# Kernel optimization log

Hardware: AMD Instinct MI355X
Metric: run time of the kernel (lower is better)

The kernel has to match this reference:

```python
import jax, jax.numpy as jnp
import numpy as np

WINDOW_SIZE = 2
SOFTMAX_TEMP = 0.01
CART_RESOLUTION = 0.25
RANGE_KEEP = 3.0
EPS = 1e-12


def get_indices(batch_size, window_size):
    kp, dense = [], []
    for i in range(batch_size):
        for j in range(window_size - 1):
            kp.append(i * window_size + j)
            dense.append(i * window_size + j + 1)
    return np.asarray(kp), np.asarray(dense)


def normalize_coords(coords, height, width):
    # coords [B,N,2] pixel (u,v) -> [-1,1] (align_corners=True convention, as in the repo)
    u = 2.0 * coords[..., 0] / (width - 1) - 1.0
    v = 2.0 * coords[..., 1] / (height - 1) - 1.0
    return jnp.stack([u, v], axis=-1)


def grid_sample_bilinear(img, grid):
    # Matches torch F.grid_sample(mode='bilinear', padding_mode='zeros', align_corners=False)
    # img [B,C,H,W], grid [B,Hg,Wg,2] with (x,y) in [-1,1]
    B, C, H, W = img.shape
    x = ((grid[..., 0] + 1.0) * W - 1.0) * 0.5
    y = ((grid[..., 1] + 1.0) * H - 1.0) * 0.5
    x0 = jnp.floor(x); y0 = jnp.floor(y)
    wx1 = x - x0; wy1 = y - y0

    def gather(xi, yi):
        valid = (xi >= 0) & (xi <= W - 1) & (yi >= 0) & (yi <= H - 1)
        xc = jnp.clip(xi, 0, W - 1).astype(jnp.int32)
        yc = jnp.clip(yi, 0, H - 1).astype(jnp.int32)
        v = jax.vmap(lambda im, yy, xx: im[:, yy, xx])(img, yc, xc)  # [B,C,Hg,Wg]
        return v * valid[:, None].astype(img.dtype)

    x1 = x0 + 1.0; y1 = y0 + 1.0
    out = (gather(x0, y0) * ((1.0 - wx1) * (1.0 - wy1))[:, None]
           + gather(x1, y0) * (wx1 * (1.0 - wy1))[:, None]
           + gather(x0, y1) * ((1.0 - wx1) * wy1)[:, None]
           + gather(x1, y1) * (wx1 * wy1)[:, None])
    return out


def setup_inputs() -> dict:
    key = jax.random.key(0)
    k1, k2, k3, k4, k5 = jax.random.split(key, 5)
    BW, C, N, H, W = 4, 256, 1024, 256, 256
    return {
        "keypoint_scores": jax.random.uniform(k1, (BW, 1, N), jnp.float32),
        "keypoint_desc": jax.random.normal(k2, (BW, C, N), jnp.float32),
        "scores_dense": jax.random.uniform(k3, (BW, 1, H, W), jnp.float32),
        "desc_dense": jax.random.normal(k4, (BW, C, H, W), jnp.float32),
        "keypoint_coords": jax.random.uniform(k5, (BW, N, 2), jnp.float32) * (W - 1),
    }


def reference(keypoint_scores, keypoint_desc, scores_dense, desc_dense, keypoint_coords):
    BW, encoder_dim, n_points = keypoint_desc.shape
    batch_size = BW // WINDOW_SIZE
    _, _, height, width = desc_dense.shape
    kp_inds, dense_inds = get_indices(batch_size, WINDOW_SIZE)

    src_coords = keypoint_coords[kp_inds]                      # [B,N,2]
    src_desc = keypoint_desc[kp_inds]                          # [B,C,N]
    src_desc = src_desc / jnp.maximum(jnp.linalg.norm(src_desc, axis=1, keepdims=True), EPS)
    B = src_desc.shape[0]

    tgt_desc_dense = desc_dense[dense_inds]                    # [B,C,H,W]
    tgt = tgt_desc_dense.reshape(B, encoder_dim, height * width)
    tgt = tgt / jnp.maximum(jnp.linalg.norm(tgt, axis=1, keepdims=True), EPS)

    # dense correlation [B, n_points, H*W]
    match_vals = jnp.einsum('bcn,bcm->bnm', src_desc, tgt)

    # local window mask (vectorized equivalent of the B x n_points python loop)
    keep_range = int(RANGE_KEEP // CART_RESOLUTION + 1)
    uv = jax.lax.stop_gradient(jnp.trunc(src_coords)).astype(jnp.int32)  # [B,N,2]
    u = uv[..., 0][..., None]   # [B,N,1]
    v = uv[..., 1][..., None]
    vg = jnp.arange(height)[None, None, :]
    ug = jnp.arange(width)[None, None, :]
    vmask = (vg >= v - keep_range) & (vg <= v + keep_range)    # [B,N,H]
    umask = (ug >= u - keep_range) & (ug <= u + keep_range)    # [B,N,W]
    mask = (vmask[..., :, None] & umask[..., None, :]).reshape(B, n_points, height * width)
    match_vals = match_vals * mask.astype(match_vals.dtype)

    soft = jax.nn.softmax(match_vals / SOFTMAX_TEMP, axis=2)   # [B,N,HW]

    # soft-argmax over the dense grid (meshgrid 'ij': v over rows, u over cols)
    ucoord = jnp.tile(jnp.arange(width, dtype=jnp.float32), height)
    vcoord = jnp.repeat(jnp.arange(height, dtype=jnp.float32), width)
    coords = jnp.stack([ucoord, vcoord], axis=1)               # [HW,2]
    pseudo_coords = jnp.einsum('bnm,mc->bnc', soft, coords)    # [B,N,2]

    pseudo_norm = normalize_coords(pseudo_coords, height, width)[:, None]  # [B,1,N,2]

    tgt_scores_dense = scores_dense[dense_inds]                # [B,1,H,W]
    pseudo_scores = grid_sample_bilinear(tgt_scores_dense, pseudo_norm).reshape(B, 1, n_points)
    pseudo_desc = grid_sample_bilinear(tgt_desc_dense, pseudo_norm).reshape(B, encoder_dim, n_points)

    desc_match_score = jnp.sum(src_desc * pseudo_desc, axis=1, keepdims=True) / float(encoder_dim)
    src_scores = keypoint_scores[kp_inds]
    match_weights = 0.5 * (desc_match_score + 1.0) * src_scores * pseudo_scores  # score_comp=True

    return pseudo_coords, match_weights, jnp.asarray(kp_inds)
```

## Files before the change

kernel.cpp:

```cpp
#include <hip/hip_runtime.h>
#include <math.h>

#define HH 256
#define WW 256
#define CC 256
#define HW 65536
#define NPTS 1024
#define BB 2
#define KEEP 13
#define KEEPM 14
#define TINV 100.0f
#define EPSN 1e-12f
#define S_ALL 8355840.0f

#define TW 32
#define TH 4
#define TUN 8
#define TPB 512
#define NT  (BB * TPB)
#define CAPT 192
#define VSTRIDE 864
#define BPAD 36
#define KPB 64

__global__ __launch_bounds__(256) void prep_src(const float* __restrict__ kdesc,
                                                const float* __restrict__ kcoords,
                                                float* __restrict__ srcn,
                                                unsigned int* __restrict__ kparams) {
    __shared__ float tr[KPB][CC + 1];
    __shared__ float red[4][KPB];
    __shared__ float s_inv[KPB];
    int t = threadIdx.x;
    int kpt0 = blockIdx.x * KPB;
    int b = kpt0 >> 10;
    int n0 = kpt0 & 1023;
    const float* srcbase = kdesc + (size_t)(2 * b) * CC * NPTS;

    int cj = t >> 6, nj = t & 63;
    for (int c0 = 0; c0 < CC; c0 += 4)
        tr[nj][c0 + cj] = srcbase[(size_t)(c0 + cj) * NPTS + n0 + nj];
    __syncthreads();

    {
        int j = t & 63, p = t >> 6;
        float ss = 0.f;
#pragma unroll 8
        for (int i = 0; i < 64; i++) {
            float x = tr[j][p * 64 + i];
            ss = fmaf(x, x, ss);
        }
        red[p][j] = ss;
    }
    __syncthreads();
    if (t < KPB) {
        float ss = red[0][t] + red[1][t] + red[2][t] + red[3][t];
        s_inv[t] = 1.0f / fmaxf(sqrtf(ss), EPSN);
        int kpt = kpt0 + t;
        int n = kpt & 1023;
        float cu = kcoords[((size_t)(2 * b) * NPTS + n) * 2 + 0];
        float cv = kcoords[((size_t)(2 * b) * NPTS + n) * 2 + 1];
        int u = (int)truncf(cu), v = (int)truncf(cv);
        int u0m = max(0, u - KEEPM), u1m = min(WW - 1, u + KEEPM);
        int v0m = max(0, v - KEEPM), v1m = min(HH - 1, v + KEEPM);
        int nWm = u1m - u0m + 1, nHm = v1m - v0m + 1;
        kparams[kpt] = (unsigned)u0m | ((unsigned)v0m << 8) |
                       ((unsigned)nWm << 16) | ((unsigned)nHm << 24);
    }
    __syncthreads();
    for (int j = 0; j < KPB; j++)
        srcn[(size_t)(kpt0 + j) * CC + t] = tr[j][t] * s_inv[j];
}

__global__ __launch_bounds__(256) void corr_tiles(const float* __restrict__ ddense,
                                                  const float* __restrict__ srcn,
                                                  const unsigned int* __restrict__ kparams,
                                                  float* __restrict__ vals,
                                                  float* __restrict__ invn) {
    __shared__ __align__(16) float B_lds[CC][BPAD];
    __shared__ float s_inorm[TW * TH];
    __shared__ int s_kid[CAPT];
    __shared__ unsigned int s_kp[CAPT];
    __shared__ int s_cnt;

    int tileg = blockIdx.x;
    int b = tileg >> 9, tl = tileg & 511;
    int tv = tl >> 3, tu = tl & 7;
    int vb = tv * TH, ub = tu * TW;
    int t = threadIdx.x;
    if (t == 0) s_cnt = 0;
    __syncthreads();

    for (int i = t; i < NPTS; i += 256) {
        unsigned int kp = kparams[b * NPTS + i];
        int u0m = kp & 255, v0m = (kp >> 8) & 255;
        int nWm = (kp >> 16) & 255, nHm = (int)(kp >> 24);
        if (u0m <= ub + TW - 1 && u0m + nWm - 1 >= ub &&
            v0m <= vb + TH - 1 && v0m + nHm - 1 >= vb) {
            int slot = atomicAdd(&s_cnt, 1);
            if (slot < CAPT) {
                s_kid[slot] = b * NPTS + i;
                s_kp[slot] = kp;
            }
        }
    }
    __syncthreads();
    int nk = min(s_cnt, CAPT);
    if (nk == 0) return;

    int pxg = t & 31, kg = t >> 5;
    int px4 = pxg * 4, k4 = kg * 4;
    int wv = vb + (px4 >> 5), wu0 = ub + (px4 & 31);
    const float* abase = ddense + (size_t)(2 * b + 1) * CC * HW +
                         (size_t)wv * WW + wu0;

    for (int kc = 0; kc < nk; kc += 32) {
        int nkk = min(32, nk - kc);
#pragma unroll 4
        for (int i = 0; i < nkk; i++)
            B_lds[t][i] = srcn[(size_t)s_kid[kc + i] * CC + t];
        __syncthreads();

        float acc[4][4];
#pragma unroll
        for (int i = 0; i < 4; i++)
#pragma unroll
            for (int j = 0; j < 4; j++) acc[i][j] = 0.f;

        int kgn = (nkk + 3) >> 2;
        if (kg < kgn) {
            float ss0 = 0.f, ss1 = 0.f, ss2 = 0.f, ss3 = 0.f;
#pragma unroll 4
            for (int c = 0; c < CC; c++) {
                float4 av = *(const float4*)(abase + (size_t)c * HW);
                const float* brow = &B_lds[c][k4];
                float b0 = brow[0], b1 = brow[1], b2 = brow[2], b3 = brow[3];
                acc[0][0] = fmaf(av.x, b0, acc[0][0]);
                acc[0][1] = fmaf(av.x, b1, acc[0][1]);
                acc[0][2] = fmaf(av.x, b2, acc[0][2]);
                acc[0][3] = fmaf(av.x, b3, acc[0][3]);
                acc[1][0] = fmaf(av.y, b0, acc[1][0]);
                acc[1][1] = fmaf(av.y, b1, acc[1][1]);
                acc[1][2] = fmaf(av.y, b2, acc[1][2]);
                acc[1][3] = fmaf(av.y, b3, acc[1][3]);
                acc[2][0] = fmaf(av.z, b0, acc[2][0]);
                acc[2][1] = fmaf(av.z, b1, acc[2][1]);
                acc[2][2] = fmaf(av.z, b2, acc[2][2]);
                acc[2][3] = fmaf(av.z, b3, acc[2][3]);
                acc[3][0] = fmaf(av.w, b0, acc[3][0]);
                acc[3][1] = fmaf(av.w, b1, acc[3][1]);
                acc[3][2] = fmaf(av.w, b2, acc[3][2]);
                acc[3][3] = fmaf(av.w, b3, acc[3][3]);
                ss0 = fmaf(av.x, av.x, ss0);
                ss1 = fmaf(av.y, av.y, ss1);
                ss2 = fmaf(av.z, av.z, ss2);
                ss3 = fmaf(av.w, av.w, ss3);
            }
            if (kc == 0 && kg == 0) {
                float i0 = 1.0f / fmaxf(sqrtf(ss0), EPSN);
                float i1 = 1.0f / fmaxf(sqrtf(ss1), EPSN);
                float i2 = 1.0f / fmaxf(sqrtf(ss2), EPSN);
                float i3 = 1.0f / fmaxf(sqrtf(ss3), EPSN);
                s_inorm[px4 + 0] = i0;
                s_inorm[px4 + 1] = i1;
                s_inorm[px4 + 2] = i2;
                s_inorm[px4 + 3] = i3;
                float* ip = invn + (size_t)b * HW + wv * WW + wu0;
                ip[0] = i0; ip[1] = i1; ip[2] = i2; ip[3] = i3;
            }
        }
        if (kc == 0) __syncthreads();

#pragma unroll
        for (int i = 0; i < 4; i++) {
            int px = px4 + i;
            int swv = vb + (px >> 5), swu = ub + (px & 31);
            float iv = s_inorm[px];
#pragma unroll
            for (int j = 0; j < 4; j++) {
                int s = k4 + j;
                if (s < nkk) {
                    unsigned int kp = s_kp[kc + s];
                    int u0m = kp & 255, v0m = (kp >> 8) & 255;
                    int nWm = (kp >> 16) & 255, nHm = (int)(kp >> 24);
                    int du = swu - u0m, dv = swv - v0m;
                    if ((unsigned)du < (unsigned)nWm && (unsigned)dv < (unsigned)nHm)
                        vals[(size_t)s_kid[kc + s] * VSTRIDE + dv * nWm + du] =
                            acc[i][j] * iv;
                }
            }
        }
        __syncthreads();
    }
}

__device__ inline float blockSum(float v, float* sred, int t) {
    for (int o = 32; o > 0; o >>= 1) v += __shfl_down(v, o, 64);
    __syncthreads();
    if ((t & 63) == 0) sred[t >> 6] = v;
    __syncthreads();
    return sred[0] + sred[1] + sred[2] + sred[3];
}

__global__ __launch_bounds__(256) void finish(const float* __restrict__ kscores,
                                              const float* __restrict__ sdense,
                                              const float* __restrict__ ddense,
                                              const float* __restrict__ kcoords,
                                              const float* __restrict__ srcn,
                                              const float* __restrict__ vals,
                                              const float* __restrict__ invn,
                                              float* __restrict__ out) {
    __shared__ float s_src[CC];
    __shared__ float s_red[4];
    int t = threadIdx.x;
    int kpt = blockIdx.x;
    int b = kpt >> 10, n = kpt & 1023;

    s_src[t] = srcn[(size_t)kpt * CC + t];

    float cu = kcoords[((size_t)(2 * b) * NPTS + n) * 2 + 0];
    float cv = kcoords[((size_t)(2 * b) * NPTS + n) * 2 + 1];
    int u = (int)truncf(cu), v = (int)truncf(cv);
    int u0 = max(0, u - KEEP), u1 = min(WW - 1, u + KEEP);
    int v0 = max(0, v - KEEP), v1 = min(HH - 1, v + KEEP);
    int nW = u1 - u0 + 1, nH = v1 - v0 + 1;
    int cnt = nW * nH;
    int u0m = max(0, u - KEEPM), u1m = min(WW - 1, u + KEEPM);
    int v0m = max(0, v - KEEPM), v1m = min(HH - 1, v + KEEPM);
    int nWm = u1m - u0m + 1, nHm = v1m - v0m + 1;
    int cntm = nWm * nHm;

    const float* vrow = vals + (size_t)kpt * VSTRIDE;
    __syncthreads();

    float valk[4];
    int puk[4], pvk[4];
    bool gk[4];
    float lm = -INFINITY;
#pragma unroll
    for (int k = 0; k < 4; k++) {
        int p = t + k * 256;
        bool gm = p < cntm;
        int pp = gm ? p : 0;
        int dvm = pp / nWm, dum = pp - dvm * nWm;
        int pu = u0m + dum, pv = v0m + dvm;
        bool inw = gm && pu >= u0 && pu <= u1 && pv >= v0 && pv <= v1;
        float val = inw ? vrow[pp] : 0.f;
        valk[k] = val;
        puk[k] = pu;
        pvk[k] = pv;
        gk[k] = inw;
        if (inw) lm = fmaxf(lm, val);
    }

    for (int o = 32; o > 0; o >>= 1) lm = fmaxf(lm, __shfl_down(lm, o, 64));
    if ((t & 63) == 0) s_red[t >> 6] = lm;
    __syncthreads();
    float m = fmaxf(fmaxf(s_red[0], s_red[1]), fmaxf(s_red[2], s_red[3]));
    m = fmaxf(m, 0.0f);

    float pse = 0.f, psu = 0.f, psv = 0.f;
#pragma unroll
    for (int k = 0; k < 4; k++) {
        float e = gk[k] ? expf(TINV * (valk[k] - m)) : 0.f;
        pse += e;
        psu = fmaf(e, (float)puk[k], psu);
        psv = fmaf(e, (float)pvk[k], psv);
    }
    float se = blockSum(pse, s_red, t);
    float su = blockSum(psu, s_red, t);
    float sv = blockSum(psv, s_red, t);

    float em = expf(-TINV * m);
    float sumWinU = 0.5f * (float)(u0 + u1) * (float)nW * (float)nH;
    float sumWinV = 0.5f * (float)(v0 + v1) * (float)nH * (float)nW;
    float denom = se + (65536.0f - (float)cnt) * em;
    float pcu = (su + em * (S_ALL - sumWinU)) / denom;
    float pcv = (sv + em * (S_ALL - sumWinV)) / denom;

    if (t == 0) {
        out[((size_t)b * NPTS + n) * 2 + 0] = pcu;
        out[((size_t)b * NPTS + n) * 2 + 1] = pcv;
    }

    float x = pcu * (256.0f / 255.0f) - 0.5f;
    float y = pcv * (256.0f / 255.0f) - 0.5f;
    float x0f = floorf(x), y0f = floorf(y);
    float wx = x - x0f, wy = y - y0f;
    int xi0 = (int)x0f, yi0 = (int)y0f, xi1 = xi0 + 1, yi1 = yi0 + 1;
    float w00 = (1.f - wx) * (1.f - wy), w10 = wx * (1.f - wy);
    float w01 = (1.f - wx) * wy, w11 = wx * wy;
    bool vx0 = (xi0 >= 0) & (xi0 < WW), vx1 = (xi1 >= 0) & (xi1 < WW);
    bool vy0 = (yi0 >= 0) & (yi0 < HH), vy1 = (yi1 >= 0) & (yi1 < HH);
    int cx0 = min(max(xi0, 0), WW - 1), cx1 = min(max(xi1, 0), WW - 1);
    int cy0 = min(max(yi0, 0), HH - 1), cy1 = min(max(yi1, 0), HH - 1);

    int cxs[4] = {cx0, cx1, cx0, cx1};
    int cys[4] = {cy0, cy0, cy1, cy1};
    bool cvalid[4] = {vx0 && vy0, vx1 && vy0, vx0 && vy1, vx1 && vy1};
    float wts[4] = {w00, w10, w01, w11};

    bool need = false;
    float dacc = 0.f;
#pragma unroll
    for (int c4 = 0; c4 < 4; c4++) {
        if (cvalid[c4]) {
            int du = cxs[c4] - u0m, dv = cys[c4] - v0m;
            if ((unsigned)du < (unsigned)nWm && (unsigned)dv < (unsigned)nHm) {
                float inv = invn[(size_t)b * HW + cys[c4] * WW + cxs[c4]];
                dacc = fmaf(wts[c4], vrow[dv * nWm + du] / inv, dacc);
            } else {
                need = true;
            }
        }
    }

    float dms;
    if (need) {
        const float* tgt = ddense + (size_t)(2 * b + 1) * CC * HW;
        int c = t;
        const float* ch = tgt + ((size_t)c << 16);
        float d00 = cvalid[0] ? ch[cys[0] * WW + cxs[0]] : 0.f;
        float d10 = cvalid[1] ? ch[cys[1] * WW + cxs[1]] : 0.f;
        float d01 = cvalid[2] ? ch[cys[2] * WW + cxs[2]] : 0.f;
        float d11 = cvalid[3] ? ch[cys[3] * WW + cxs[3]] : 0.f;
        float pd = d00 * wts[0] + d10 * wts[1] + d01 * wts[2] + d11 * wts[3];
        float dsum = blockSum(pd * s_src[c], s_red, t);
        dms = dsum / (float)CC;
    } else {
        dms = dacc / (float)CC;
    }

    if (t == 0) {
        const float* sch = sdense + (size_t)(2 * b + 1) * HW;
        float s00 = cvalid[0] ? sch[cys[0] * WW + cxs[0]] : 0.f;
        float s10 = cvalid[1] ? sch[cys[1] * WW + cxs[1]] : 0.f;
        float s01 = cvalid[2] ? sch[cys[2] * WW + cxs[2]] : 0.f;
        float s11 = cvalid[3] ? sch[cys[3] * WW + cxs[3]] : 0.f;
        float psc = s00 * wts[0] + s10 * wts[1] + s01 * wts[2] + s11 * wts[3];
        float sscore = kscores[(size_t)(2 * b) * NPTS + n];
        float wgt = 0.5f * (dms + 1.0f) * sscore * psc;
        out[2 * NPTS * BB + (size_t)b * NPTS + n] = wgt;
    }

    if (kpt == 0 && t < 2) out[3 * NPTS * BB + t] = 2.0f * (float)t;
}

__global__ __launch_bounds__(256) void prep_tgt(const float* __restrict__ dd,
                                                float* __restrict__ invn) {
    int idx = blockIdx.x * 256 + threadIdx.x;
    int b = idx >> 16, m = idx & 65535;
    const float* p = dd + (size_t)(2 * b + 1) * CC * HW + m;
    float ss = 0.f;
#pragma unroll 4
    for (int c = 0; c < CC; c++) {
        float x = p[(size_t)c << 16];
        ss += x * x;
    }
    invn[idx] = 1.0f / fmaxf(sqrtf(ss), EPSN);
}

__global__ __launch_bounds__(256) void matcher(const float* __restrict__ kscores,
                                               const float* __restrict__ sdense,
                                               const float* __restrict__ ddense,
                                               const float* __restrict__ kcoords,
                                               const float* __restrict__ srcn,
                                               const float* __restrict__ invn,
                                               float* __restrict__ out) {
    __shared__ float s_src[CC];
    __shared__ float s_red[4];
    int t = threadIdx.x;
    int kpt = blockIdx.x;
    int b = kpt >> 10, n = kpt & 1023;

    s_src[t] = srcn[(size_t)kpt * CC + t];

    float cu = kcoords[((size_t)(2 * b) * NPTS + n) * 2 + 0];
    float cv = kcoords[((size_t)(2 * b) * NPTS + n) * 2 + 1];
    int u = (int)truncf(cu), v = (int)truncf(cv);
    int u0 = max(0, u - KEEP), u1 = min(WW - 1, u + KEEP);
    int v0 = max(0, v - KEEP), v1 = min(HH - 1, v + KEEP);
    int nW = u1 - u0 + 1, nH = v1 - v0 + 1;
    int cnt = nW * nH;

    const float* tgt = ddense + (size_t)(2 * b + 1) * CC * HW;
    const float* inb = invn + (size_t)b * HW;
    __syncthreads();

    int p0 = t, p1 = t + 256, p2 = t + 512;
    bool g0 = p0 < cnt, g1 = p1 < cnt, g2 = p2 < cnt;
    int dv0 = p0 / nW, dv1 = p1 / nW, dv2 = p2 / nW;
    int uu0 = u0 + (p0 - dv0 * nW), uu1 = u0 + (p1 - dv1 * nW), uu2 = u0 + (p2 - dv2 * nW);
    int vv0 = v0 + dv0, vv1 = v0 + dv1, vv2 = v0 + dv2;
    int mi0 = g0 ? (vv0 * WW + uu0) : 0;
    int mi1 = g1 ? (vv1 * WW + uu1) : 0;
    int mi2 = g2 ? (vv2 * WW + uu2) : 0;

    const float* q0 = tgt + mi0;
    const float* q1 = tgt + mi1;
    const float* q2 = tgt + mi2;
    float a0 = 0.f, a1 = 0.f, a2 = 0.f;
#pragma unroll 4
    for (int c = 0; c < CC; c++) {
        float s = s_src[c];
        size_t off = (size_t)c << 16;
        a0 = fmaf(s, q0[off], a0);
        a1 = fmaf(s, q1[off], a1);
        a2 = fmaf(s, q2[off], a2);
    }
    float val0 = a0 * inb[mi0];
    float val1 = a1 * inb[mi1];
    float val2 = a2 * inb[mi2];

    float lm = fmaxf(fmaxf(g0 ? val0 : -INFINITY, g1 ? val1 : -INFINITY),
                     g2 ? val2 : -INFINITY);
    for (int o = 32; o > 0; o >>= 1) lm = fmaxf(lm, __shfl_down(lm, o, 64));
    if ((t & 63) == 0) s_red[t >> 6] = lm;
    __syncthreads();
    float m = fmaxf(fmaxf(s_red[0], s_red[1]), fmaxf(s_red[2], s_red[3]));
    m = fmaxf(m, 0.0f);

    float e0 = g0 ? expf(TINV * (val0 - m)) : 0.f;
    float e1 = g1 ? expf(TINV * (val1 - m)) : 0.f;
    float e2 = g2 ? expf(TINV * (val2 - m)) : 0.f;

    float se = blockSum(e0 + e1 + e2, s_red, t);
    float su = blockSum(e0 * uu0 + e1 * uu1 + e2 * uu2, s_red, t);
    float sv = blockSum(e0 * vv0 + e1 * vv1 + e2 * vv2, s_red, t);

    float em = expf(-TINV * m);
    float sumWinU = 0.5f * (float)(u0 + u1) * (float)nW * (float)nH;
    float sumWinV = 0.5f * (float)(v0 + v1) * (float)nH * (float)nW;
    float denom = se + (65536.0f - (float)cnt) * em;
    float pcu = (su + em * (S_ALL - sumWinU)) / denom;
    float pcv = (sv + em * (S_ALL - sumWinV)) / denom;

    if (t == 0) {
        out[((size_t)b * NPTS + n) * 2 + 0] = pcu;
        out[((size_t)b * NPTS + n) * 2 + 1] = pcv;
    }

    float x = pcu * (256.0f / 255.0f) - 0.5f;
    float y = pcv * (256.0f / 255.0f) - 0.5f;
    float x0f = floorf(x), y0f = floorf(y);
    float wx = x - x0f, wy = y - y0f;
    int xi0 = (int)x0f, yi0 = (int)y0f, xi1 = xi0 + 1, yi1 = yi0 + 1;
    float w00 = (1.f - wx) * (1.f - wy), w10 = wx * (1.f - wy);
    float w01 = (1.f - wx) * wy, w11 = wx * wy;
    bool vx0 = (xi0 >= 0) & (xi0 < WW), vx1 = (xi1 >= 0) & (xi1 < WW);
    bool vy0 = (yi0 >= 0) & (yi0 < HH), vy1 = (yi1 >= 0) & (yi1 < HH);
    int cx0 = min(max(xi0, 0), WW - 1), cx1 = min(max(xi1, 0), WW - 1);
    int cy0 = min(max(yi0, 0), HH - 1), cy1 = min(max(yi1, 0), HH - 1);

    {
        int c = t;
        const float* ch = tgt + ((size_t)c << 16);
        float d00 = (vx0 && vy0) ? ch[cy0 * WW + cx0] : 0.f;
        float d10 = (vx1 && vy0) ? ch[cy0 * WW + cx1] : 0.f;
        float d01 = (vx0 && vy1) ? ch[cy1 * WW + cx0] : 0.f;
        float d11 = (vx1 && vy1) ? ch[cy1 * WW + cx1] : 0.f;
        float pd = d00 * w00 + d10 * w10 + d01 * w01 + d11 * w11;
        float contrib = pd * s_src[c];
        float dsum = blockSum(contrib, s_red, t);
        if (t == 0) {
            float dms = dsum / (float)CC;
            const float* sch = sdense + (size_t)(2 * b + 1) * HW;
            float s00 = (vx0 && vy0) ? sch[cy0 * WW + cx0] : 0.f;
            float s10 = (vx1 && vy0) ? sch[cy0 * WW + cx1] : 0.f;
            float s01 = (vx0 && vy1) ? sch[cy1 * WW + cx0] : 0.f;
            float s11 = (vx1 && vy1) ? sch[cy1 * WW + cx1] : 0.f;
            float psc = s00 * w00 + s10 * w10 + s01 * w01 + s11 * w11;
            float sscore = kscores[(size_t)(2 * b) * NPTS + n];
            float wgt = 0.5f * (dms + 1.0f) * sscore * psc;
            out[2 * NPTS * BB + (size_t)b * NPTS + n] = wgt;
        }
    }

    if (kpt == 0 && t < 2) out[3 * NPTS * BB + t] = 2.0f * (float)t;
}

extern "C" void kernel_launch(void* const* d_in, const int* in_sizes, int n_in,
                              void* d_out, int out_size, void* d_ws, size_t ws_size,
                              hipStream_t stream) {
    const float* kscores = (const float*)d_in[0];
    const float* kdesc   = (const float*)d_in[1];
    const float* sdense  = (const float*)d_in[2];
    const float* ddense  = (const float*)d_in[3];
    const float* kcoords = (const float*)d_in[4];
    float* out = (float*)d_out;

    float* srcn = (float*)d_ws;
    float* vals = srcn + (size_t)BB * NPTS * CC;
    float* invn = vals + (size_t)BB * NPTS * VSTRIDE;
    unsigned int* kparams = (unsigned int*)(invn + (size_t)BB * HW);
    size_t need = ((size_t)BB * NPTS * CC + (size_t)BB * NPTS * VSTRIDE +
                   (size_t)BB * HW + BB * NPTS) * 4;

    if (ws_size >= need) {
        hipLaunchKernelGGL(prep_src, dim3(BB * NPTS / KPB), dim3(256), 0, stream,
                           kdesc, kcoords, srcn, kparams);
        hipLaunchKernelGGL(corr_tiles, dim3(NT), dim3(256), 0, stream,
                           ddense, srcn, kparams, vals, invn);
        hipLaunchKernelGGL(finish, dim3(BB * NPTS), dim3(256), 0, stream,
                           kscores, sdense, ddense, kcoords, srcn, vals, invn, out);
    } else {
        float* invn2 = srcn + (size_t)BB * NPTS * CC;
        hipLaunchKernelGGL(prep_src, dim3(BB * NPTS / KPB), dim3(256), 0, stream,
                           kdesc, kcoords, srcn, kparams);
        hipLaunchKernelGGL(prep_tgt, dim3(512), dim3(256), 0, stream, ddense, invn2);
        hipLaunchKernelGGL(matcher, dim3(BB * NPTS), dim3(256), 0, stream,
                           kscores, sdense, ddense, kcoords, srcn, invn2, out);
    }
}
```

Before: 91.92 us.

## Split channel reduction across wave halves with 4x8 register tile per thread

Measured after the change: 84.47 us. 8.1% less time.

```diff
diff --git a/kernel.cpp b/kernel.cpp
--- a/kernel.cpp
+++ b/kernel.cpp
@@ -107,85 +107,122 @@
     int nk = min(s_cnt, CAPT);
     if (nk == 0) return;
 
-    int pxg = t & 31, kg = t >> 5;
-    int px4 = pxg * 4, k4 = kg * 4;
+    int lane = t & 63;
+    int half = lane >> 5;
+    int pxg = lane & 31;
+    int kg = t >> 6;
+    int k8 = kg * 8;
+    int px4 = pxg * 4;
     int wv = vb + (px4 >> 5), wu0 = ub + (px4 & 31);
     const float* abase = ddense + (size_t)(2 * b + 1) * CC * HW +
-                         (size_t)wv * WW + wu0;
+                         (size_t)half * HW + (size_t)wv * WW + wu0;
 
     for (int kc = 0; kc < nk; kc += 32) {
         int nkk = min(32, nk - kc);
 #pragma unroll 4
         for (int i = 0; i < nkk; i++)
             B_lds[t][i] = srcn[(size_t)s_kid[kc + i] * CC + t];
+        for (int i = nkk; i < 32; i++) B_lds[t][i] = 0.f;
         __syncthreads();
 
-        float acc[4][4];
+        float acc[4][8];
 #pragma unroll
         for (int i = 0; i < 4; i++)
 #pragma unroll
-            for (int j = 0; j < 4; j++) acc[i][j] = 0.f;
-
-        int kgn = (nkk + 3) >> 2;
+            for (int j = 0; j < 8; j++) acc[i][j] = 0.f;
+
+        int kgn = (nkk + 7) >> 3;
         if (kg < kgn) {
             float ss0 = 0.f, ss1 = 0.f, ss2 = 0.f, ss3 = 0.f;
+            bool dos = (kg == 0) && (kc == 0);
 #pragma unroll 4
-            for (int c = 0; c < CC; c++) {
-                float4 av = *(const float4*)(abase + (size_t)c * HW);
-                const float* brow = &B_lds[c][k4];
+            for (int cc = 0; cc < CC / 2; cc++) {
+                float4 av = *(const float4*)(abase + (size_t)cc * (2 * HW));
+                const float* brow = &B_lds[2 * cc + half][k8];
                 float b0 = brow[0], b1 = brow[1], b2 = brow[2], b3 = brow[3];
+                float b4 = brow[4], b5 = brow[5], b6 = brow[6], b7 = brow[7];
                 acc[0][0] = fmaf(av.x, b0, acc[0][0]);
                 acc[0][1] = fmaf(av.x, b1, acc[0][1]);
                 acc[0][2] = fmaf(av.x, b2, acc[0][2]);
                 acc[0][3] = fmaf(av.x, b3, acc[0][3]);
+                acc[0][4] = fmaf(av.x, b4, acc[0][4]);
+                acc[0][5] = fmaf(av.x, b5, acc[0][5]);
+                acc[0][6] = fmaf(av.x, b6, acc[0][6]);
+                acc[0][7] = fmaf(av.x, b7, acc[0][7]);
                 acc[1][0] = fmaf(av.y, b0, acc[1][0]);
                 acc[1][1] = fmaf(av.y, b1, acc[1][1]);
                 acc[1][2] = fmaf(av.y, b2, acc[1][2]);
                 acc[1][3] = fmaf(av.y, b3, acc[1][3]);
+                acc[1][4] = fmaf(av.y, b4, acc[1][4]);
+                acc[1][5] = fmaf(av.y, b5, acc[1][5]);
+                acc[1][6] = fmaf(av.y, b6, acc[1][6]);
+                acc[1][7] = fmaf(av.y, b7, acc[1][7]);
                 acc[2][0] = fmaf(av.z, b0, acc[2][0]);
                 acc[2][1] = fmaf(av.z, b1, acc[2][1]);
                 acc[2][2] = fmaf(av.z, b2, acc[2][2]);
                 acc[2][3] = fmaf(av.z, b3, acc[2][3]);
+                acc[2][4] = fmaf(av.z, b4, acc[2][4]);
+                acc[2][5] = fmaf(av.z, b5, acc[2][5]);
+                acc[2][6] = fmaf(av.z, b6, acc[2][6]);
+                acc[2][7] = fmaf(av.z, b7, acc[2][7]);
                 acc[3][0] = fmaf(av.w, b0, acc[3][0]);
                 acc[3][1] = fmaf(av.w, b1, acc[3][1]);
                 acc[3][2] = fmaf(av.w, b2, acc[3][2]);
                 acc[3][3] = fmaf(av.w, b3, acc[3][3]);
-                ss0 = fmaf(av.x, av.x, ss0);
-                ss1 = fmaf(av.y, av.y, ss1);
-                ss2 = fmaf(av.z, av.z, ss2);
-                ss3 = fmaf(av.w, av.w, ss3);
+                acc[3][4] = fmaf(av.w, b4, acc[3][4]);
+                acc[3][5] = fmaf(av.w, b5, acc[3][5]);
+                acc[3][6] = fmaf(av.w, b6, acc[3][6]);
+                acc[3][7] = fmaf(av.w, b7, acc[3][7]);
+                if (dos) {
+                    ss0 = fmaf(av.x, av.x, ss0);
+                    ss1 = fmaf(av.y, av.y, ss1);
+                    ss2 = fmaf(av.z, av.z, ss2);
+                    ss3 = fmaf(av.w, av.w, ss3);
+                }
             }
-            if (kc == 0 && kg == 0) {
-                float i0 = 1.0f / fmaxf(sqrtf(ss0), EPSN);
-                float i1 = 1.0f / fmaxf(sqrtf(ss1), EPSN);
-                float i2 = 1.0f / fmaxf(sqrtf(ss2), EPSN);
-                float i3 = 1.0f / fmaxf(sqrtf(ss3), EPSN);
-                s_inorm[px4 + 0] = i0;
-                s_inorm[px4 + 1] = i1;
-                s_inorm[px4 + 2] = i2;
-                s_inorm[px4 + 3] = i3;
-                float* ip = invn + (size_t)b * HW + wv * WW + wu0;
-                ip[0] = i0; ip[1] = i1; ip[2] = i2; ip[3] = i3;
+#pragma unroll
+            for (int i = 0; i < 4; i++)
+#pragma unroll
+                for (int j = 0; j < 8; j++)
+                    acc[i][j] += __shfl_xor(acc[i][j], 32, 64);
+            if (dos) {
+                ss0 += __shfl_xor(ss0, 32, 64);
+                ss1 += __shfl_xor(ss1, 32, 64);
+                ss2 += __shfl_xor(ss2, 32, 64);
+                ss3 += __shfl_xor(ss3, 32, 64);
+                if (half == 0) {
+                    float i0 = 1.0f / fmaxf(sqrtf(ss0), EPSN);
+                    float i1 = 1.0f / fmaxf(sqrtf(ss1), EPSN);
+                    float i2 = 1.0f / fmaxf(sqrtf(ss2), EPSN);
+                    float i3 = 1.0f / fmaxf(sqrtf(ss3), EPSN);
+                    s_inorm[px4 + 0] = i0;
+                    s_inorm[px4 + 1] = i1;
+                    s_inorm[px4 + 2] = i2;
+                    s_inorm[px4 + 3] = i3;
+                    float* ip = invn + (size_t)b * HW + wv * WW + wu0;
+                    ip[0] = i0; ip[1] = i1; ip[2] = i2; ip[3] = i3;
+                }
             }
         }
         if (kc == 0) __syncthreads();
 
-#pragma unroll
-        for (int i = 0; i < 4; i++) {
-            int px = px4 + i;
-            int swv = vb + (px >> 5), swu = ub + (px & 31);
-            float iv = s_inorm[px];
-#pragma unroll
-            for (int j = 0; j < 4; j++) {
-                int s = k4 + j;
-                if (s < nkk) {
-                    unsigned int kp = s_kp[kc + s];
-                    int u0m = kp & 255, v0m = (kp >> 8) & 255;
-                    int nWm = (kp >> 16) & 255, nHm = (int)(kp >> 24);
-                    int du = swu - u0m, dv = swv - v0m;
-                    if ((unsigned)du < (unsigned)nWm && (unsigned)dv < (unsigned)nHm)
-                        vals[(size_t)s_kid[kc + s] * VSTRIDE + dv * nWm + du] =
-                            acc[i][j] * iv;
+        if (half == 0) {
+#pragma unroll
+            for (int i = 0; i < 4; i++) {
+                int swu = wu0 + i;
+                float iv = s_inorm[px4 + i];
+#pragma unroll
+                for (int j = 0; j < 8; j++) {
+                    int s = k8 + j;
+                    if (s < nkk) {
+                        unsigned int kp = s_kp[kc + s];
+                        int u0m = kp & 255, v0m = (kp >> 8) & 255;
+                        int nWm = (kp >> 16) & 255, nHm = (int)(kp >> 24);
+                        int du = swu - u0m, dv = wv - v0m;
+                        if ((unsigned)du < (unsigned)nWm && (unsigned)dv < (unsigned)nHm)
+                            vals[(size_t)s_kid[kc + s] * VSTRIDE + dv * nWm + du] =
+                                acc[i][j] * iv;
+                    }
                 }
             }
         }
```
